# Performance work log

Hardware: AMD Instinct MI355X
Metric: run time of the kernel (lower is better)

Reference implementation:

```python
import jax, jax.numpy as jnp
import numpy as np

EPS = 1e-5


def setup_inputs() -> dict:
    key = jax.random.key(0)
    k1, k2, k3, k4 = jax.random.split(key, 4)
    B, C, H, W = 4, 64, 128, 256
    Hg, Wg = 512, 1024
    NC = 19  # num_class; loop also covers ignore label 255 -> NC+1 entries
    x = jax.random.normal(k1, (B, C, H, W), dtype=jnp.float32)
    gt = jax.random.randint(k2, (B, Hg, Wg), 0, 19).astype(jnp.int32)
    eps_mu = jax.random.normal(k3, (NC + 1, B, C), dtype=jnp.float32)
    eps_std = jax.random.normal(k4, (NC + 1, B, C), dtype=jnp.float32)
    return {"x": x, "gt": gt, "eps_mu": eps_mu, "eps_std": eps_std}


def _sqrtvar(t):
    # torch .var(dim=0) is unbiased (ddof=1); repeat over batch is just broadcast
    return jnp.sqrt(jnp.var(t, axis=0, ddof=1, keepdims=True) + EPS)


def reference(x, gt, eps_mu, eps_std):
    B, C, H, W = x.shape
    NC1 = eps_mu.shape[0]  # num_class + 1 (ignore label 255)
    Hg, Wg = gt.shape[1], gt.shape[2]
    # nearest resize of the (binary) mask == compare on nearest-resized labels
    # torch F.interpolate nearest: src = floor(dst * in/out)
    ih = (jnp.arange(H) * Hg) // H
    iw = (jnp.arange(W) * Wg) // W
    gt_r = gt[:, ih[:, None], iw[None, :]]  # [B,H,W]
    class_ids = jnp.concatenate(
        [jnp.arange(NC1 - 1), jnp.array([255])]).astype(gt.dtype)

    def per_class(carry, inp):
        cid, emu, estd = inp
        mask = (gt_r == cid).astype(x.dtype)[:, None]  # [B,1,H,W]
        mx = x * mask
        npx = jnp.sum(mask, axis=(2, 3))               # [B,1]
        npx = jnp.where(npx == 0, jnp.ones_like(npx), npx)
        mean = jnp.sum(mx, axis=(2, 3)) / npx          # [B,C] == mean*wh/npx
        var = jnp.sum((mask * (mx - mean[:, :, None, None])) ** 2,
                      axis=(2, 3)) / npx
        std = jnp.sqrt(var + EPS)                      # [B,C]
        beta = mean + emu * _sqrtvar(mean)
        gamma = std + estd * _sqrtvar(std)
        xn = (mx - mean[:, :, None, None]) / std[:, :, None, None]
        out = mask * (xn * gamma[:, :, None, None] + beta[:, :, None, None])
        return carry + out, None

    class_x, _ = jax.lax.scan(per_class, jnp.zeros_like(x),
                              (class_ids, eps_mu, eps_std))
    return class_x
```

## Files before the change

kernel.cpp:

```cpp
#include <hip/hip_runtime.h>

#define EPS 1e-5f
constexpr int B = 4, C = 64, H = 128, W = 256;
constexpr int Hg = 512, Wg = 1024;
constexpr int NC = 19;
constexpr int HW = H * W;

__global__ __launch_bounds__(256) void k_downsample(const int* __restrict__ gt,
                                                    int* __restrict__ gt_r,
                                                    int* __restrict__ counts) {
  __shared__ int hist[NC];
  int t = threadIdx.x;
  if (t < NC) hist[t] = 0;
  __syncthreads();
  int blk = blockIdx.x;
  int b = blk >> 7;
  int h = blk & (H - 1);
  int cls = gt[(size_t)(b * Hg + h * 4) * Wg + t * 4];
  gt_r[blk * W + t] = cls;
  if ((unsigned)cls < (unsigned)NC) atomicAdd(&hist[cls], 1);
  __syncthreads();
  if (t < NC && hist[t] != 0) atomicAdd(&counts[b * NC + t], hist[t]);
}

__global__ __launch_bounds__(256) void k_stats(const float* __restrict__ x,
                                               const int* __restrict__ gt_r,
                                               float* __restrict__ sums,
                                               float* __restrict__ sqs) {
  __shared__ float accS[NC * 256];
  __shared__ float accQ[NC * 256];
  int t = threadIdx.x;
  for (int k = t; k < NC * 256; k += 256) { accS[k] = 0.f; accQ[k] = 0.f; }
  __syncthreads();
  int bc = blockIdx.x;
  int b = bc >> 6;
  const float4* xp = (const float4*)(x + (size_t)bc * HW);
  const int4*   gp = (const int4*)(gt_r + (size_t)b * HW);
  for (int i = t; i < HW / 4; i += 256) {
    float4 v = xp[i];
    int4   g = gp[i];
    accS[g.x * 256 + t] += v.x;  accQ[g.x * 256 + t] += v.x * v.x;
    accS[g.y * 256 + t] += v.y;  accQ[g.y * 256 + t] += v.y * v.y;
    accS[g.z * 256 + t] += v.z;  accQ[g.z * 256 + t] += v.z * v.z;
    accS[g.w * 256 + t] += v.w;  accQ[g.w * 256 + t] += v.w * v.w;
  }
  for (int stride = 128; stride >= 1; stride >>= 1) {
    __syncthreads();
    if (t < stride) {
      for (int k = 0; k < NC; k++) {
        accS[k * 256 + t] += accS[k * 256 + t + stride];
        accQ[k * 256 + t] += accQ[k * 256 + t + stride];
      }
    }
  }
  __syncthreads();
  if (t < NC) {
    int c = bc & 63;
    sums[(t * B + b) * C + c] = accS[t * 256];
    sqs [(t * B + b) * C + c] = accQ[t * 256];
  }
}

__global__ __launch_bounds__(256) void k_params(const float* __restrict__ sums,
                                                const float* __restrict__ sqs,
                                                const int* __restrict__ counts,
                                                const float* __restrict__ eps_mu,
                                                const float* __restrict__ eps_std,
                                                float* __restrict__ scale,
                                                float* __restrict__ shift) {
  int idx = blockIdx.x * 256 + threadIdx.x;
  if (idx >= NC * C) return;
  int cid = idx / C;
  int c = idx - cid * C;
  float mean[B], stdv[B];
  float msum = 0.f, ssum = 0.f;
  for (int b = 0; b < B; b++) {
    float cnt = (float)counts[b * NC + cid];
    float n = cnt > 0.f ? cnt : 1.f;
    float s = sums[(cid * B + b) * C + c];
    float q = sqs [(cid * B + b) * C + c];
    float m = s / n;
    float var = q / n - m * m;
    var = var > 0.f ? var : 0.f;
    mean[b] = m;
    stdv[b] = sqrtf(var + EPS);
    msum += m; ssum += stdv[b];
  }
  float mbar = msum * 0.25f, sbar = ssum * 0.25f;
  float vm = 0.f, vs = 0.f;
  for (int b = 0; b < B; b++) {
    float dm = mean[b] - mbar; vm += dm * dm;
    float ds = stdv[b] - sbar; vs += ds * ds;
  }
  float sqvm = sqrtf(vm * (1.f / 3.f) + EPS);
  float sqvs = sqrtf(vs * (1.f / 3.f) + EPS);
  for (int b = 0; b < B; b++) {
    int e = (cid * B + b) * C + c;
    float beta  = mean[b] + eps_mu[e]  * sqvm;
    float gamma = stdv[b] + eps_std[e] * sqvs;
    float sc = gamma / stdv[b];
    scale[e] = sc;
    shift[e] = beta - mean[b] * sc;
  }
}

__global__ __launch_bounds__(256) void k_apply(const float* __restrict__ x,
                                               const int* __restrict__ gt_r,
                                               const float* __restrict__ scale,
                                               const float* __restrict__ shift,
                                               float* __restrict__ out) {
  __shared__ float2 tab[NC];
  int t = threadIdx.x;
  int plane = blockIdx.x >> 2;
  int quarter = blockIdx.x & 3;
  int b = plane >> 6;
  int c = plane & 63;
  if (t < NC) {
    int e = (t * B + b) * C + c;
    tab[t] = make_float2(scale[e], shift[e]);
  }
  __syncthreads();
  const float4* xp = (const float4*)(x + (size_t)plane * HW) + quarter * 2048;
  const int4*   gp = (const int4*)(gt_r + (size_t)b * HW) + quarter * 2048;
  float4*       op = (float4*)(out + (size_t)plane * HW) + quarter * 2048;
  for (int i = t; i < 2048; i += 256) {
    float4 v = xp[i];
    int4   g = gp[i];
    float2 a0 = tab[g.x], a1 = tab[g.y], a2 = tab[g.z], a3 = tab[g.w];
    float4 o;
    o.x = fmaf(v.x, a0.x, a0.y);
    o.y = fmaf(v.y, a1.x, a1.y);
    o.z = fmaf(v.z, a2.x, a2.y);
    o.w = fmaf(v.w, a3.x, a3.y);
    op[i] = o;
  }
}

extern "C" void kernel_launch(void* const* d_in, const int* in_sizes, int n_in,
                              void* d_out, int out_size, void* d_ws, size_t ws_size,
                              hipStream_t stream) {
  const float* x       = (const float*)d_in[0];
  const int*   gt      = (const int*)  d_in[1];
  const float* eps_mu  = (const float*)d_in[2];
  const float* eps_std = (const float*)d_in[3];
  float* out = (float*)d_out;

  char* ws = (char*)d_ws;
  int*   gt_r   = (int*)  (ws);
  int*   counts = (int*)  (ws + 524288);
  float* sums   = (float*)(ws + 525312);
  float* sqs    = (float*)(ws + 544768);
  float* scale  = (float*)(ws + 564224);
  float* shift  = (float*)(ws + 583680);

  hipMemsetAsync(counts, 0, NC * B * sizeof(int), stream);
  hipLaunchKernelGGL(k_downsample, dim3(B * H), dim3(W), 0, stream, gt, gt_r, counts);
  hipLaunchKernelGGL(k_stats, dim3(B * C), dim3(256), 0, stream, x, gt_r, sums, sqs);
  hipLaunchKernelGGL(k_params, dim3((NC * C + 255) / 256), dim3(256), 0, stream,
                     sums, sqs, counts, eps_mu, eps_std, scale, shift);
  hipLaunchKernelGGL(k_apply, dim3(B * C * 4), dim3(256), 0, stream,
                     x, gt_r, scale, shift, out);
}
```

Measured before the change: 124.7 us.

## Pack labels to bytes, split stats across quarters, fuse params into apply

Downsampled labels are packed four per 32-bit word, which cuts label traffic in the stats and apply passes. The stats kernel now runs four blocks per plane instead of one, uses interleaved float2 shared accumulators and a wave-shuffle reduction in place of the serial shared-memory tree. Class counts are also gathered inside the stats kernel, which removes the separate memset. The params kernel is folded into apply: each block recomputes its 19 scale/shift pairs from the quarter partials while its first tile load is in flight. This cuts launches and serial reduction work, at the cost of redundant per-block parameter math.

```diff
diff --git a/kernel.cpp b/kernel.cpp
--- a/kernel.cpp
+++ b/kernel.cpp
@@ -5,128 +5,148 @@
 constexpr int Hg = 512, Wg = 1024;
 constexpr int NC = 19;
 constexpr int HW = H * W;
+constexpr int HW4 = HW / 4;
 
-__global__ __launch_bounds__(256) void k_downsample(const int* __restrict__ gt,
-                                                    int* __restrict__ gt_r,
-                                                    int* __restrict__ counts) {
-  __shared__ int hist[NC];
+__global__ __launch_bounds__(256) void k_pack(const int* __restrict__ gt,
+                                              unsigned int* __restrict__ gt_p) {
   int t = threadIdx.x;
-  if (t < NC) hist[t] = 0;
-  __syncthreads();
-  int blk = blockIdx.x;
-  int b = blk >> 7;
-  int h = blk & (H - 1);
-  int cls = gt[(size_t)(b * Hg + h * 4) * Wg + t * 4];
-  gt_r[blk * W + t] = cls;
-  if ((unsigned)cls < (unsigned)NC) atomicAdd(&hist[cls], 1);
-  __syncthreads();
-  if (t < NC && hist[t] != 0) atomicAdd(&counts[b * NC + t], hist[t]);
+  int R = blockIdx.x * 4 + (t >> 6);
+  int ws = t & 63;
+  int b = R >> 7, h = R & 127;
+  const int* row = gt + (size_t)(b * Hg + h * 4) * Wg;
+  unsigned int c0 = (unsigned int)row[(ws * 4 + 0) * 4];
+  unsigned int c1 = (unsigned int)row[(ws * 4 + 1) * 4];
+  unsigned int c2 = (unsigned int)row[(ws * 4 + 2) * 4];
+  unsigned int c3 = (unsigned int)row[(ws * 4 + 3) * 4];
+  gt_p[R * 64 + ws] = c0 | (c1 << 8) | (c2 << 16) | (c3 << 24);
 }
 
 __global__ __launch_bounds__(256) void k_stats(const float* __restrict__ x,
-                                               const int* __restrict__ gt_r,
-                                               float* __restrict__ sums,
-                                               float* __restrict__ sqs) {
-  __shared__ float accS[NC * 256];
-  __shared__ float accQ[NC * 256];
+                                               const unsigned int* __restrict__ gt_p,
+                                               float* __restrict__ sums_p,
+                                               float* __restrict__ sqs_p,
+                                               int* __restrict__ counts_p) {
+  __shared__ float2 acc[NC * 256];
+  __shared__ int hist[NC];
   int t = threadIdx.x;
-  for (int k = t; k < NC * 256; k += 256) { accS[k] = 0.f; accQ[k] = 0.f; }
+  for (int k = t; k < NC * 256; k += 256) acc[k] = make_float2(0.f, 0.f);
+  int plane = blockIdx.x >> 2;
+  int q = blockIdx.x & 3;
+  int b = plane >> 6, c = plane & 63;
+  bool desig = (c == 0);
+  if (desig && t < NC) hist[t] = 0;
   __syncthreads();
-  int bc = blockIdx.x;
-  int b = bc >> 6;
-  const float4* xp = (const float4*)(x + (size_t)bc * HW);
-  const int4*   gp = (const int4*)(gt_r + (size_t)b * HW);
-  for (int i = t; i < HW / 4; i += 256) {
+
+  const float4* xp = (const float4*)x + (size_t)plane * (HW / 4) + q * 2048;
+  const unsigned int* gp = gt_p + (size_t)b * HW4 + q * 2048;
+  for (int j = 0; j < 8; j++) {
+    int i = j * 256 + t;
     float4 v = xp[i];
-    int4   g = gp[i];
-    accS[g.x * 256 + t] += v.x;  accQ[g.x * 256 + t] += v.x * v.x;
-    accS[g.y * 256 + t] += v.y;  accQ[g.y * 256 + t] += v.y * v.y;
-    accS[g.z * 256 + t] += v.z;  accQ[g.z * 256 + t] += v.z * v.z;
-    accS[g.w * 256 + t] += v.w;  accQ[g.w * 256 + t] += v.w * v.w;
-  }
-  for (int stride = 128; stride >= 1; stride >>= 1) {
-    __syncthreads();
-    if (t < stride) {
-      for (int k = 0; k < NC; k++) {
-        accS[k * 256 + t] += accS[k * 256 + t + stride];
-        accQ[k * 256 + t] += accQ[k * 256 + t + stride];
-      }
+    unsigned int g = gp[i];
+    int c0 = g & 255, c1 = (g >> 8) & 255, c2 = (g >> 16) & 255, c3 = g >> 24;
+    float2 a;
+    a = acc[c0 * 256 + t]; a.x += v.x; a.y += v.x * v.x; acc[c0 * 256 + t] = a;
+    a = acc[c1 * 256 + t]; a.x += v.y; a.y += v.y * v.y; acc[c1 * 256 + t] = a;
+    a = acc[c2 * 256 + t]; a.x += v.z; a.y += v.z * v.z; acc[c2 * 256 + t] = a;
+    a = acc[c3 * 256 + t]; a.x += v.w; a.y += v.w * v.w; acc[c3 * 256 + t] = a;
+    if (desig) {
+      atomicAdd(&hist[c0], 1); atomicAdd(&hist[c1], 1);
+      atomicAdd(&hist[c2], 1); atomicAdd(&hist[c3], 1);
     }
   }
   __syncthreads();
-  if (t < NC) {
-    int c = bc & 63;
-    sums[(t * B + b) * C + c] = accS[t * 256];
-    sqs [(t * B + b) * C + c] = accQ[t * 256];
+
+  int w = t >> 6, lane = t & 63;
+  for (int k = w; k < NC; k += 4) {
+    float2 a0 = acc[k * 256 + lane];
+    float2 a1 = acc[k * 256 + 64 + lane];
+    float2 a2 = acc[k * 256 + 128 + lane];
+    float2 a3 = acc[k * 256 + 192 + lane];
+    float s  = a0.x + a1.x + a2.x + a3.x;
+    float qq = a0.y + a1.y + a2.y + a3.y;
+    for (int m = 32; m >= 1; m >>= 1) {
+      s  += __shfl_xor(s, m, 64);
+      qq += __shfl_xor(qq, m, 64);
+    }
+    if (lane == 0) {
+      int e = (k * B + b) * C + c;
+      sums_p[e * 4 + q] = s;
+      sqs_p [e * 4 + q] = qq;
+    }
   }
-}
-
-__global__ __launch_bounds__(256) void k_params(const float* __restrict__ sums,
-                                                const float* __restrict__ sqs,
-                                                const int* __restrict__ counts,
-                                                const float* __restrict__ eps_mu,
-                                                const float* __restrict__ eps_std,
-                                                float* __restrict__ scale,
-                                                float* __restrict__ shift) {
-  int idx = blockIdx.x * 256 + threadIdx.x;
-  if (idx >= NC * C) return;
-  int cid = idx / C;
-  int c = idx - cid * C;
-  float mean[B], stdv[B];
-  float msum = 0.f, ssum = 0.f;
-  for (int b = 0; b < B; b++) {
-    float cnt = (float)counts[b * NC + cid];
-    float n = cnt > 0.f ? cnt : 1.f;
-    float s = sums[(cid * B + b) * C + c];
-    float q = sqs [(cid * B + b) * C + c];
-    float m = s / n;
-    float var = q / n - m * m;
-    var = var > 0.f ? var : 0.f;
-    mean[b] = m;
-    stdv[b] = sqrtf(var + EPS);
-    msum += m; ssum += stdv[b];
-  }
-  float mbar = msum * 0.25f, sbar = ssum * 0.25f;
-  float vm = 0.f, vs = 0.f;
-  for (int b = 0; b < B; b++) {
-    float dm = mean[b] - mbar; vm += dm * dm;
-    float ds = stdv[b] - sbar; vs += ds * ds;
-  }
-  float sqvm = sqrtf(vm * (1.f / 3.f) + EPS);
-  float sqvs = sqrtf(vs * (1.f / 3.f) + EPS);
-  for (int b = 0; b < B; b++) {
-    int e = (cid * B + b) * C + c;
-    float beta  = mean[b] + eps_mu[e]  * sqvm;
-    float gamma = stdv[b] + eps_std[e] * sqvs;
-    float sc = gamma / stdv[b];
-    scale[e] = sc;
-    shift[e] = beta - mean[b] * sc;
-  }
+  if (desig && t < NC) counts_p[(b * NC + t) * 4 + q] = hist[t];
 }
 
 __global__ __launch_bounds__(256) void k_apply(const float* __restrict__ x,
-                                               const int* __restrict__ gt_r,
-                                               const float* __restrict__ scale,
-                                               const float* __restrict__ shift,
+                                               const unsigned int* __restrict__ gt_p,
+                                               const float* __restrict__ sums_p,
+                                               const float* __restrict__ sqs_p,
+                                               const int* __restrict__ counts_p,
+                                               const float* __restrict__ eps_mu,
+                                               const float* __restrict__ eps_std,
                                                float* __restrict__ out) {
   __shared__ float2 tab[NC];
   int t = threadIdx.x;
   int plane = blockIdx.x >> 2;
-  int quarter = blockIdx.x & 3;
-  int b = plane >> 6;
-  int c = plane & 63;
+  int q = blockIdx.x & 3;
+  int b = plane >> 6, c = plane & 63;
+  const float4* xp = (const float4*)x + (size_t)plane * (HW / 4) + q * 2048;
+  const unsigned int* gp = gt_p + (size_t)b * HW4 + q * 2048;
+  float4* op = (float4*)out + (size_t)plane * (HW / 4) + q * 2048;
+
+  float4 v0 = xp[t];
+  unsigned int g0 = gp[t];
+
   if (t < NC) {
+    float mean[B], stdv[B];
+    float msum = 0.f, ssum = 0.f;
+    for (int bb = 0; bb < B; bb++) {
+      int4 cn = *(const int4*)&counts_p[(bb * NC + t) * 4];
+      float n = (float)(cn.x + cn.y + cn.z + cn.w);
+      if (n == 0.f) n = 1.f;
+      float4 s4 = *(const float4*)&sums_p[((t * B + bb) * C + c) * 4];
+      float4 q4 = *(const float4*)&sqs_p [((t * B + bb) * C + c) * 4];
+      float s  = s4.x + s4.y + s4.z + s4.w;
+      float qq = q4.x + q4.y + q4.z + q4.w;
+      float m = s / n;
+      float var = qq / n - m * m;
+      var = var > 0.f ? var : 0.f;
+      mean[bb] = m;
+      stdv[bb] = sqrtf(var + EPS);
+      msum += m; ssum += stdv[bb];
+    }
+    float mbar = msum * 0.25f, sbar = ssum * 0.25f;
+    float vm = 0.f, vs = 0.f;
+    for (int bb = 0; bb < B; bb++) {
+      float dm = mean[bb] - mbar; vm += dm * dm;
+      float ds = stdv[bb] - sbar; vs += ds * ds;
+    }
+    float sqvm = sqrtf(vm * (1.f / 3.f) + EPS);
+    float sqvs = sqrtf(vs * (1.f / 3.f) + EPS);
     int e = (t * B + b) * C + c;
-    tab[t] = make_float2(scale[e], shift[e]);
+    float beta  = mean[b] + eps_mu[e]  * sqvm;
+    float gamma = stdv[b] + eps_std[e] * sqvs;
+    float sc = gamma / stdv[b];
+    tab[t] = make_float2(sc, beta - mean[b] * sc);
   }
   __syncthreads();
-  const float4* xp = (const float4*)(x + (size_t)plane * HW) + quarter * 2048;
-  const int4*   gp = (const int4*)(gt_r + (size_t)b * HW) + quarter * 2048;
-  float4*       op = (float4*)(out + (size_t)plane * HW) + quarter * 2048;
-  for (int i = t; i < 2048; i += 256) {
+
+  {
+    float2 a0 = tab[g0 & 255], a1 = tab[(g0 >> 8) & 255];
+    float2 a2 = tab[(g0 >> 16) & 255], a3 = tab[g0 >> 24];
+    float4 o;
+    o.x = fmaf(v0.x, a0.x, a0.y);
+    o.y = fmaf(v0.y, a1.x, a1.y);
+    o.z = fmaf(v0.z, a2.x, a2.y);
+    o.w = fmaf(v0.w, a3.x, a3.y);
+    op[t] = o;
+  }
+  for (int j = 1; j < 8; j++) {
+    int i = j * 256 + t;
     float4 v = xp[i];
-    int4   g = gp[i];
-    float2 a0 = tab[g.x], a1 = tab[g.y], a2 = tab[g.z], a3 = tab[g.w];
+    unsigned int g = gp[i];
+    float2 a0 = tab[g & 255], a1 = tab[(g >> 8) & 255];
+    float2 a2 = tab[(g >> 16) & 255], a3 = tab[g >> 24];
     float4 o;
     o.x = fmaf(v.x, a0.x, a0.y);
     o.y = fmaf(v.y, a1.x, a1.y);
@@ -146,18 +166,14 @@
   float* out = (float*)d_out;
 
   char* ws = (char*)d_ws;
-  int*   gt_r   = (int*)  (ws);
-  int*   counts = (int*)  (ws + 524288);
-  float* sums   = (float*)(ws + 525312);
-  float* sqs    = (float*)(ws + 544768);
-  float* scale  = (float*)(ws + 564224);
-  float* shift  = (float*)(ws + 583680);
+  unsigned int* gt_p    = (unsigned int*)(ws);
+  float*        sums_p  = (float*)(ws + 131072);
+  float*        sqs_p   = (float*)(ws + 208896);
+  int*          counts_p= (int*)  (ws + 286720);
 
-  hipMemsetAsync(counts, 0, NC * B * sizeof(int), stream);
-  hipLaunchKernelGGL(k_downsample, dim3(B * H), dim3(W), 0, stream, gt, gt_r, counts);
-  hipLaunchKernelGGL(k_stats, dim3(B * C), dim3(256), 0, stream, x, gt_r, sums, sqs);
-  hipLaunchKernelGGL(k_params, dim3((NC * C + 255) / 256), dim3(256), 0, stream,
-                     sums, sqs, counts, eps_mu, eps_std, scale, shift);
+  hipLaunchKernelGGL(k_pack,  dim3(B * H / 4), dim3(256), 0, stream, gt, gt_p);
+  hipLaunchKernelGGL(k_stats, dim3(B * C * 4), dim3(256), 0, stream,
+                     x, gt_p, sums_p, sqs_p, counts_p);
   hipLaunchKernelGGL(k_apply, dim3(B * C * 4), dim3(256), 0, stream,
-                     x, gt_r, scale, shift, out);
+                     x, gt_p, sums_p, sqs_p, counts_p, eps_mu, eps_std, out);
 }
```

After: 105.6 us. 1.18x faster.
